# Kernel tuning notes

Hardware: AMD Instinct MI355X
Metric: run time of the kernel (lower is better)

Reference implementation:

```python
import jax, jax.numpy as jnp
import numpy as np

N_CAND = 10   # n_point_candidate
SIGMA = 1.0   # std threshold for vote filtering
EPS = 1e-6


def _get_pt_candidates(pcld, kpts_ofst, seg, cpt_ofst, k):
    # pcld [b,n,3]; kpts_ofst [b,n,8,3]; seg [b,n,1]; cpt_ofst [b,n,1,3]
    offsets = jnp.concatenate([kpts_ofst, cpt_ofst], axis=2)        # [b,n,9,3]
    scores = jnp.squeeze(seg, axis=-1)                              # [b,n]
    _, idx = jax.lax.top_k(scores, k)                               # [b,k] most confident points
    cands = pcld[:, :, None, :] + offsets                           # [b,n,9,3] candidate kpt positions
    cands = jnp.take_along_axis(cands, idx[:, :, None, None], axis=1)  # [b,k,9,3]
    return jnp.transpose(cands, (0, 2, 1, 3))                       # [b,9,k,3]


def _pts_clustering_with_std(kpts_cans, sigma=SIGMA):
    # kpts_cans [b,n_kpts,k,3]: keep candidates within sigma*std of the mean, average survivors
    mean = jnp.mean(kpts_cans, axis=2, keepdims=True)
    std = jnp.std(kpts_cans, axis=2, keepdims=True)
    inlier = jnp.all(jnp.abs(kpts_cans - mean) <= sigma * std, axis=-1)  # [b,n_kpts,k]
    w = inlier.astype(kpts_cans.dtype)[..., None]
    return jnp.sum(kpts_cans * w, axis=2) / (jnp.sum(w, axis=2) + EPS)   # [b,n_kpts,3]


def _rt_svd_transform(A, B, w):
    # Weighted Kabsch: find R,t with R @ A + t ~= B.  A,B [b,n,3]; w [n]
    wn = w / jnp.sum(w)
    cA = jnp.einsum('n,bnc->bc', wn, A)[:, None, :]                 # weighted centroids
    cB = jnp.einsum('n,bnc->bc', wn, B)[:, None, :]
    Am, Bm = A - cA, B - cB
    H = jnp.einsum('bni,n,bnj->bij', Am, w, Bm)                     # [b,3,3] cross-covariance
    U, S, Vh = jnp.linalg.svd(H)
    V = jnp.swapaxes(Vh, -1, -2)
    R0 = V @ jnp.swapaxes(U, -1, -2)
    flip = jnp.where(jnp.linalg.det(R0) < 0.0, -1.0, 1.0)           # reflection fix
    V = V.at[:, :, -1].multiply(flip[:, None])
    R = V @ jnp.swapaxes(U, -1, -2)                                 # [b,3,3]
    t = jnp.swapaxes(cB, -1, -2) - R @ jnp.swapaxes(cA, -1, -2)     # [b,3,1]
    return R, t


def setup_inputs() -> dict:
    key = jax.random.key(0)
    k1, k2, k3, k4, k5 = jax.random.split(key, 5)
    b, n, nk = 64, 12288, 8
    return {
        'pcld_input': jax.random.normal(k1, (b, n, 3), jnp.float32),
        'kpts_pre_input': jax.random.normal(k2, (b, n, nk, 3), jnp.float32),
        'cpt_pre_input': jax.random.normal(k3, (b, n, 1, 3), jnp.float32),
        'seg_pre_input': jax.random.uniform(k4, (b, n, 1), jnp.float32),
        'mesh_kpts_input': jax.random.normal(k5, (b, nk + 1, 3), jnp.float32),
    }


def reference(pcld_input, kpts_pre_input, cpt_pre_input, seg_pre_input, mesh_kpts_input):
    obj_kpts = _get_pt_candidates(pcld_input, kpts_pre_input, seg_pre_input, cpt_pre_input, N_CAND)
    kpts_voted = _pts_clustering_with_std(obj_kpts)                 # [b,9,3]
    n_pts = kpts_voted.shape[1]
    weights_vector = jnp.ones((n_pts,), dtype=kpts_voted.dtype)
    batch_R, batch_t = _rt_svd_transform(mesh_kpts_input, kpts_voted, weights_vector)
    batch_t = jnp.reshape(batch_t, (-1, 3))
    return batch_R, batch_t, kpts_voted
```

## Files before the change

kernel.cpp:

```cpp
#include <hip/hip_runtime.h>
#include <math.h>

typedef unsigned long long u64;
typedef unsigned int u32;

#define NB      64
#define NPTS    12288
#define KTOP    10
#define NKP     9
#define T       1024
#define CAND_MAX 128
#define THETA   0.997f

#define CHUNKS   4
#define TPB_A    768
#define CAP      64
#define TPB_B    128
#define WS_STRIDE 320

__device__ __forceinline__ u64 pack(float v, int idx) {
    return ((u64)__float_as_uint(v) << 32) | (u32)(~idx);
}
__device__ __forceinline__ int unpack_idx(u64 p) { return (int)(~(u32)p); }

__device__ __forceinline__ float rcp_fast(float x)  { return __builtin_amdgcn_rcpf(x); }
__device__ __forceinline__ float rsq_fast(float x)  { return __builtin_amdgcn_rsqf(x); }
__device__ __forceinline__ float sqrt_fast(float x) { return __builtin_amdgcn_sqrtf(x); }

__global__ __launch_bounds__(TPB_A)
void pose_filter(const float* __restrict__ seg, u64* __restrict__ ws)
{
    const int blk   = blockIdx.x;
    const int b     = blk >> 2;
    const int chunk = blk & 3;
    const int t     = threadIdx.x;

    __shared__ u64 lc[CAP];
    __shared__ int lcnt;
    if (t == 0) lcnt = 0;
    __syncthreads();

    const float4* segc4 = (const float4*)(seg + (size_t)b * NPTS) + (size_t)chunk * TPB_A;
    float4 a = segc4[t];
    const int base_idx = chunk * (TPB_A * 4) + t * 4;
    #pragma unroll
    for (int c = 0; c < 4; ++c) {
        float v = (c == 0) ? a.x : (c == 1) ? a.y : (c == 2) ? a.z : a.w;
        if (v >= THETA) {
            int slot = atomicAdd(&lcnt, 1);
            if (slot < CAP) lc[slot] = pack(v, base_idx + c);
        }
    }
    __syncthreads();

    u64* wb = ws + (size_t)b * WS_STRIDE;
    if (t == 0) wb[chunk] = (u64)lcnt;
    int m = lcnt < CAP ? lcnt : CAP;
    if (t < m) wb[4 + chunk * CAP + t] = lc[t];
}

__global__ __launch_bounds__(TPB_B)
void pose_solve(const float* __restrict__ pcld,
                const float* __restrict__ kpts,
                const float* __restrict__ cpt,
                const float* __restrict__ seg,
                const float* __restrict__ mesh,
                const u64*   __restrict__ ws,
                float* __restrict__ out)
{
    const int b = blockIdx.x;
    const int t = threadIdx.x;
    const int lane = t & 63;

    __shared__ u64    cand[CHUNKS * CAP];
    __shared__ int    n_s, bad_s;
    __shared__ int    off_s[CHUNKS];
    __shared__ int    topidx[KTOP];
    __shared__ float4 cands4[NKP][KTOP];
    __shared__ float  voted[NKP][3];
    __shared__ float  meshS[NKP * 3];

    float meshv = 0.0f;
    if (t < NKP * 3) meshv = mesh[(size_t)b * (NKP * 3) + t];

    const u64* wb = ws + (size_t)b * WS_STRIDE;
    if (t == 0) {
        int off = 0, bad = 0;
        #pragma unroll
        for (int c = 0; c < CHUNKS; ++c) {
            int cc = (int)wb[c];
            off_s[c] = off;
            off += cc;
            if (cc > CAP) bad = 1;
        }
        n_s = off;
        bad_s = bad;
    }
    if (t < NKP * 3) meshS[t] = meshv;
    __syncthreads();

    const int n = n_s;
    const int bad = bad_s;

    if (!bad) {
        #pragma unroll
        for (int c = 0; c < CHUNKS; ++c) {
            int o   = off_s[c];
            int cc  = ((c + 1 < CHUNKS) ? off_s[c + 1] : n) - o;
            if (t < cc) cand[o + t] = wb[4 + c * CAP + t];
        }
    }
    __syncthreads();

    if (!bad && n >= KTOP) {
        u64 my0 = (t < n)           ? cand[t]           : 0;
        u64 my1 = (t + TPB_B < n)   ? cand[t + TPB_B]   : 0;
        int r0 = 0, r1 = 0;
        for (int i = 0; i < n; ++i) {
            u64 ci = cand[i];
            r0 += (ci > my0) ? 1 : 0;
            r1 += (ci > my1) ? 1 : 0;
        }
        if (t < n && r0 < KTOP)         topidx[r0] = unpack_idx(my0);
        if (t + TPB_B < n && r1 < KTOP) topidx[r1] = unpack_idx(my1);
    } else if (t < 64) {
        const float* segb = seg + (size_t)b * NPTS;
        u64 loc[KTOP];
        #pragma unroll
        for (int j = 0; j < KTOP; ++j) loc[j] = 0;
        for (int i = lane; i < NPTS; i += 64) {
            u64 p = pack(segb[i], i);
            if (p > loc[KTOP - 1]) {
                loc[KTOP - 1] = p;
                #pragma unroll
                for (int j = KTOP - 1; j > 0; --j) {
                    if (loc[j] > loc[j - 1]) { u64 tmp = loc[j]; loc[j] = loc[j - 1]; loc[j - 1] = tmp; }
                }
            }
        }
        u64 cur = loc[0];
        #pragma unroll
        for (int k = 0; k < KTOP; ++k) {
            u64 w = cur;
            #pragma unroll
            for (int s = 1; s < 64; s <<= 1) {
                u64 o = __shfl_xor(w, s);
                w = o > w ? o : w;
            }
            if (lane == 0) topidx[k] = unpack_idx(w);
            if (cur == w) {
                #pragma unroll
                for (int i = 0; i + 1 < KTOP; ++i) loc[i] = loc[i + 1];
                loc[KTOP - 1] = 0;
                cur = loc[0];
            }
        }
    }
    __syncthreads();

    if (t < NKP * KTOP) {
        int j = t / KTOP;
        int i = t % KTOP;
        int p = topidx[i];
        size_t base = (size_t)b * NPTS + p;
        float px = pcld[base * 3 + 0], py = pcld[base * 3 + 1], pz = pcld[base * 3 + 2];
        float ox, oy, oz;
        if (j < 8) {
            size_t kb = (base * 8 + j) * 3;
            ox = kpts[kb + 0]; oy = kpts[kb + 1]; oz = kpts[kb + 2];
        } else {
            size_t cb = base * 3;
            ox = cpt[cb + 0]; oy = cpt[cb + 1]; oz = cpt[cb + 2];
        }
        cands4[j][i] = make_float4(px + ox, py + oy, pz + oz, 0.0f);
    }
    __syncthreads();

    if (t < NKP) {
        float4 c4[KTOP];
        #pragma unroll
        for (int i = 0; i < KTOP; ++i) c4[i] = cands4[t][i];

        float mean[3] = {0.f, 0.f, 0.f};
        #pragma unroll
        for (int i = 0; i < KTOP; ++i) {
            mean[0] += c4[i].x; mean[1] += c4[i].y; mean[2] += c4[i].z;
        }
        #pragma unroll
        for (int c = 0; c < 3; ++c) mean[c] *= (1.0f / KTOP);

        float var[3] = {0.f, 0.f, 0.f};
        #pragma unroll
        for (int i = 0; i < KTOP; ++i) {
            float d0 = c4[i].x - mean[0]; var[0] += d0 * d0;
            float d1 = c4[i].y - mean[1]; var[1] += d1 * d1;
            float d2 = c4[i].z - mean[2]; var[2] += d2 * d2;
        }
        float sd[3];
        #pragma unroll
        for (int c = 0; c < 3; ++c) sd[c] = sqrtf(var[c] * (1.0f / KTOP));

        float wsum = 0.f, acc[3] = {0.f, 0.f, 0.f};
        #pragma unroll
        for (int i = 0; i < KTOP; ++i) {
            bool in = (fabsf(c4[i].x - mean[0]) <= sd[0]) &&
                      (fabsf(c4[i].y - mean[1]) <= sd[1]) &&
                      (fabsf(c4[i].z - mean[2]) <= sd[2]);
            if (in) {
                wsum += 1.f;
                acc[0] += c4[i].x; acc[1] += c4[i].y; acc[2] += c4[i].z;
            }
        }
        float inv = 1.f / (wsum + 1e-6f);
        #pragma unroll
        for (int c = 0; c < 3; ++c) {
            float v = acc[c] * inv;
            voted[t][c] = v;
            out[NB * 9 + NB * 3 + ((size_t)b * NKP + t) * 3 + c] = v;
        }
    }
    __syncthreads();

    if (t == 0) {
        float A[NKP][3], Bv[NKP][3];
        float cA[3] = {0, 0, 0}, cB[3] = {0, 0, 0};
        for (int nn = 0; nn < NKP; ++nn) {
            for (int c = 0; c < 3; ++c) {
                A[nn][c]  = meshS[nn * 3 + c];
                Bv[nn][c] = voted[nn][c];
                cA[c] += A[nn][c];
                cB[c] += Bv[nn][c];
            }
        }
        for (int c = 0; c < 3; ++c) { cA[c] *= (1.0f / NKP); cB[c] *= (1.0f / NKP); }

        float H[3][3] = {{0,0,0},{0,0,0},{0,0,0}};
        for (int nn = 0; nn < NKP; ++nn)
            for (int i = 0; i < 3; ++i)
                for (int j = 0; j < 3; ++j)
                    H[i][j] += (A[nn][i] - cA[i]) * (Bv[nn][j] - cB[j]);

        float Km[3][3];
        for (int i = 0; i < 3; ++i)
            for (int j = 0; j < 3; ++j) {
                float s = 0;
                for (int l = 0; l < 3; ++l) s += H[l][i] * H[l][j];
                Km[i][j] = s;
            }

        float V[3][3] = {{1,0,0},{0,1,0},{0,0,1}};
        for (int sweep = 0; sweep < 5; ++sweep) {
            for (int p = 0; p < 2; ++p) {
                for (int q = p + 1; q < 3; ++q) {
                    float apq = Km[p][q];
                    float app = Km[p][p], aqq = Km[q][q];
                    if (fabsf(apq) <= 1e-12f * (fabsf(app) + fabsf(aqq)) || apq == 0.0f) continue;
                    float theta = (aqq - app) * rcp_fast(2.0f * apq);
                    float tj = ((theta >= 0.0f) ? 1.0f : -1.0f) *
                               rcp_fast(fabsf(theta) + sqrt_fast(theta * theta + 1.0f));
                    float cj = rsq_fast(tj * tj + 1.0f);
                    float sj = tj * cj;
                    for (int l = 0; l < 3; ++l) {
                        float klp = Km[l][p], klq = Km[l][q];
                        Km[l][p] = cj * klp - sj * klq;
                        Km[l][q] = sj * klp + cj * klq;
                    }
                    for (int l = 0; l < 3; ++l) {
                        float kpl = Km[p][l], kql = Km[q][l];
                        Km[p][l] = cj * kpl - sj * kql;
                        Km[q][l] = sj * kpl + cj * kql;
                    }
                    for (int l = 0; l < 3; ++l) {
                        float vlp = V[l][p], vlq = V[l][q];
                        V[l][p] = cj * vlp - sj * vlq;
                        V[l][q] = sj * vlp + cj * vlq;
                    }
                }
            }
        }

        float eig[3] = {Km[0][0], Km[1][1], Km[2][2]};
        int ord[3] = {0, 1, 2};
        if (eig[ord[0]] < eig[ord[1]]) { int tmp = ord[0]; ord[0] = ord[1]; ord[1] = tmp; }
        if (eig[ord[1]] < eig[ord[2]]) { int tmp = ord[1]; ord[1] = ord[2]; ord[2] = tmp; }
        if (eig[ord[0]] < eig[ord[1]]) { int tmp = ord[0]; ord[0] = ord[1]; ord[1] = tmp; }

        float detH =
            H[0][0] * (H[1][1] * H[2][2] - H[1][2] * H[2][1]) -
            H[0][1] * (H[1][0] * H[2][2] - H[1][2] * H[2][0]) +
            H[0][2] * (H[1][0] * H[2][1] - H[1][1] * H[2][0]);
        float dsign[3] = {1.0f, 1.0f, (detH < 0.0f) ? -1.0f : 1.0f};

        float R[3][3] = {{0,0,0},{0,0,0},{0,0,0}};
        for (int k = 0; k < 3; ++k) {
            int c = ord[k];
            float s = sqrt_fast(fmaxf(eig[c], 0.0f));
            float invs = rcp_fast(fmaxf(s, 1e-12f));
            float u[3];
            for (int l = 0; l < 3; ++l) {
                float a = 0;
                for (int m = 0; m < 3; ++m) a += H[l][m] * V[m][c];
                u[l] = a * invs;
            }
            for (int r = 0; r < 3; ++r)
                for (int cc = 0; cc < 3; ++cc)
                    R[r][cc] += dsign[k] * V[r][c] * u[cc];
        }

        float tv[3];
        for (int c = 0; c < 3; ++c) {
            float a = 0;
            for (int m = 0; m < 3; ++m) a += R[c][m] * cA[m];
            tv[c] = cB[c] - a;
        }

        for (int r = 0; r < 3; ++r)
            for (int c = 0; c < 3; ++c)
                out[(size_t)b * 9 + r * 3 + c] = R[r][c];
        for (int c = 0; c < 3; ++c)
            out[NB * 9 + (size_t)b * 3 + c] = tv[c];
    }
}

__global__ __launch_bounds__(T)
void pose_fused(const float* __restrict__ pcld,
                const float* __restrict__ kpts,
                const float* __restrict__ cpt,
                const float* __restrict__ seg,
                const float* __restrict__ mesh,
                float* __restrict__ out)
{
    const int b = blockIdx.x;
    const int t = threadIdx.x;
    const int lane = t & 63;
    const int wid = t >> 6;

    __shared__ u64    cand[CAND_MAX];
    __shared__ int    cnt;
    __shared__ int    topidx[KTOP];
    __shared__ float4 cands4[NKP][KTOP];
    __shared__ float  voted[NKP][3];
    __shared__ float  meshS[NKP * 3];

    if (t == 0) cnt = 0;
    float meshv = 0.0f;
    if (t < NKP * 3) meshv = mesh[(size_t)b * (NKP * 3) + t];
    __syncthreads();

    const float4* segb4 = (const float4*)(seg + (size_t)b * NPTS);
    #pragma unroll
    for (int j = 0; j < 3; ++j) {
        int f4 = t + j * T;
        float4 a = segb4[f4];
        #pragma unroll
        for (int c = 0; c < 4; ++c) {
            float v = (c == 0) ? a.x : (c == 1) ? a.y : (c == 2) ? a.z : a.w;
            if (v >= THETA) {
                int slot = atomicAdd(&cnt, 1);
                if (slot < CAND_MAX) cand[slot] = pack(v, 4 * f4 + c);
            }
        }
    }
    if (t < NKP * 3) meshS[t] = meshv;
    __syncthreads();

    if (wid == 0) {
        int n = cnt;
        if (n >= KTOP && n <= CAND_MAX) {
            u64 my0 = (lane < n)      ? cand[lane]      : 0;
            u64 my1 = (lane + 64 < n) ? cand[lane + 64] : 0;
            int r0 = 0, r1 = 0;
            for (int i = 0; i < n; ++i) {
                u64 ci = cand[i];
                r0 += (ci > my0) ? 1 : 0;
                r1 += (ci > my1) ? 1 : 0;
            }
            if (lane < n && r0 < KTOP)      topidx[r0] = unpack_idx(my0);
            if (lane + 64 < n && r1 < KTOP) topidx[r1] = unpack_idx(my1);
        } else {
            const float* segb = seg + (size_t)b * NPTS;
            u64 loc[KTOP];
            #pragma unroll
            for (int j = 0; j < KTOP; ++j) loc[j] = 0;
            for (int i = lane; i < NPTS; i += 64) {
                u64 p = pack(segb[i], i);
                if (p > loc[KTOP - 1]) {
                    loc[KTOP - 1] = p;
                    #pragma unroll
                    for (int j = KTOP - 1; j > 0; --j) {
                        if (loc[j] > loc[j - 1]) { u64 tmp = loc[j]; loc[j] = loc[j - 1]; loc[j - 1] = tmp; }
                    }
                }
            }
            u64 cur = loc[0];
            #pragma unroll
            for (int k = 0; k < KTOP; ++k) {
                u64 w = cur;
                #pragma unroll
                for (int s = 1; s < 64; s <<= 1) {
                    u64 o = __shfl_xor(w, s);
                    w = o > w ? o : w;
                }
                if (lane == 0) topidx[k] = unpack_idx(w);
                if (cur == w) {
                    #pragma unroll
                    for (int i = 0; i + 1 < KTOP; ++i) loc[i] = loc[i + 1];
                    loc[KTOP - 1] = 0;
                    cur = loc[0];
                }
            }
        }
    }
    __syncthreads();

    if (t < NKP * KTOP) {
        int j = t / KTOP;
        int i = t % KTOP;
        int p = topidx[i];
        size_t base = (size_t)b * NPTS + p;
        float px = pcld[base * 3 + 0], py = pcld[base * 3 + 1], pz = pcld[base * 3 + 2];
        float ox, oy, oz;
        if (j < 8) {
            size_t kb = (base * 8 + j) * 3;
            ox = kpts[kb + 0]; oy = kpts[kb + 1]; oz = kpts[kb + 2];
        } else {
            size_t cb = base * 3;
            ox = cpt[cb + 0]; oy = cpt[cb + 1]; oz = cpt[cb + 2];
        }
        cands4[j][i] = make_float4(px + ox, py + oy, pz + oz, 0.0f);
    }
    __syncthreads();

    if (t < NKP) {
        float4 c4[KTOP];
        #pragma unroll
        for (int i = 0; i < KTOP; ++i) c4[i] = cands4[t][i];
        float mean[3] = {0.f, 0.f, 0.f};
        #pragma unroll
        for (int i = 0; i < KTOP; ++i) { mean[0] += c4[i].x; mean[1] += c4[i].y; mean[2] += c4[i].z; }
        #pragma unroll
        for (int c = 0; c < 3; ++c) mean[c] *= (1.0f / KTOP);
        float var[3] = {0.f, 0.f, 0.f};
        #pragma unroll
        for (int i = 0; i < KTOP; ++i) {
            float d0 = c4[i].x - mean[0]; var[0] += d0 * d0;
            float d1 = c4[i].y - mean[1]; var[1] += d1 * d1;
            float d2 = c4[i].z - mean[2]; var[2] += d2 * d2;
        }
        float sd[3];
        #pragma unroll
        for (int c = 0; c < 3; ++c) sd[c] = sqrtf(var[c] * (1.0f / KTOP));
        float wsum = 0.f, acc[3] = {0.f, 0.f, 0.f};
        #pragma unroll
        for (int i = 0; i < KTOP; ++i) {
            bool in = (fabsf(c4[i].x - mean[0]) <= sd[0]) &&
                      (fabsf(c4[i].y - mean[1]) <= sd[1]) &&
                      (fabsf(c4[i].z - mean[2]) <= sd[2]);
            if (in) { wsum += 1.f; acc[0] += c4[i].x; acc[1] += c4[i].y; acc[2] += c4[i].z; }
        }
        float inv = 1.f / (wsum + 1e-6f);
        #pragma unroll
        for (int c = 0; c < 3; ++c) {
            float v = acc[c] * inv;
            voted[t][c] = v;
            out[NB * 9 + NB * 3 + ((size_t)b * NKP + t) * 3 + c] = v;
        }
    }
    __syncthreads();

    if (t == 0) {
        float A[NKP][3], Bv[NKP][3];
        float cA[3] = {0, 0, 0}, cB[3] = {0, 0, 0};
        for (int nn = 0; nn < NKP; ++nn) {
            for (int c = 0; c < 3; ++c) {
                A[nn][c]  = meshS[nn * 3 + c];
                Bv[nn][c] = voted[nn][c];
                cA[c] += A[nn][c];
                cB[c] += Bv[nn][c];
            }
        }
        for (int c = 0; c < 3; ++c) { cA[c] *= (1.0f / NKP); cB[c] *= (1.0f / NKP); }
        float H[3][3] = {{0,0,0},{0,0,0},{0,0,0}};
        for (int nn = 0; nn < NKP; ++nn)
            for (int i = 0; i < 3; ++i)
                for (int j = 0; j < 3; ++j)
                    H[i][j] += (A[nn][i] - cA[i]) * (Bv[nn][j] - cB[j]);
        float Km[3][3];
        for (int i = 0; i < 3; ++i)
            for (int j = 0; j < 3; ++j) {
                float s = 0;
                for (int l = 0; l < 3; ++l) s += H[l][i] * H[l][j];
                Km[i][j] = s;
            }
        float V[3][3] = {{1,0,0},{0,1,0},{0,0,1}};
        for (int sweep = 0; sweep < 5; ++sweep) {
            for (int p = 0; p < 2; ++p) {
                for (int q = p + 1; q < 3; ++q) {
                    float apq = Km[p][q];
                    float app = Km[p][p], aqq = Km[q][q];
                    if (fabsf(apq) <= 1e-12f * (fabsf(app) + fabsf(aqq)) || apq == 0.0f) continue;
                    float theta = (aqq - app) * rcp_fast(2.0f * apq);
                    float tj = ((theta >= 0.0f) ? 1.0f : -1.0f) *
                               rcp_fast(fabsf(theta) + sqrt_fast(theta * theta + 1.0f));
                    float cj = rsq_fast(tj * tj + 1.0f);
                    float sj = tj * cj;
                    for (int l = 0; l < 3; ++l) {
                        float klp = Km[l][p], klq = Km[l][q];
                        Km[l][p] = cj * klp - sj * klq;
                        Km[l][q] = sj * klp + cj * klq;
                    }
                    for (int l = 0; l < 3; ++l) {
                        float kpl = Km[p][l], kql = Km[q][l];
                        Km[p][l] = cj * kpl - sj * kql;
                        Km[q][l] = sj * kpl + cj * kql;
                    }
                    for (int l = 0; l < 3; ++l) {
                        float vlp = V[l][p], vlq = V[l][q];
                        V[l][p] = cj * vlp - sj * vlq;
                        V[l][q] = sj * vlp + cj * vlq;
                    }
                }
            }
        }
        float eig[3] = {Km[0][0], Km[1][1], Km[2][2]};
        int ord[3] = {0, 1, 2};
        if (eig[ord[0]] < eig[ord[1]]) { int tmp = ord[0]; ord[0] = ord[1]; ord[1] = tmp; }
        if (eig[ord[1]] < eig[ord[2]]) { int tmp = ord[1]; ord[1] = ord[2]; ord[2] = tmp; }
        if (eig[ord[0]] < eig[ord[1]]) { int tmp = ord[0]; ord[0] = ord[1]; ord[1] = tmp; }
        float detH =
            H[0][0] * (H[1][1] * H[2][2] - H[1][2] * H[2][1]) -
            H[0][1] * (H[1][0] * H[2][2] - H[1][2] * H[2][0]) +
            H[0][2] * (H[1][0] * H[2][1] - H[1][1] * H[2][0]);
        float dsign[3] = {1.0f, 1.0f, (detH < 0.0f) ? -1.0f : 1.0f};
        float R[3][3] = {{0,0,0},{0,0,0},{0,0,0}};
        for (int k = 0; k < 3; ++k) {
            int c = ord[k];
            float s = sqrt_fast(fmaxf(eig[c], 0.0f));
            float invs = rcp_fast(fmaxf(s, 1e-12f));
            float u[3];
            for (int l = 0; l < 3; ++l) {
                float a = 0;
                for (int m = 0; m < 3; ++m) a += H[l][m] * V[m][c];
                u[l] = a * invs;
            }
            for (int r = 0; r < 3; ++r)
                for (int cc = 0; cc < 3; ++cc)
                    R[r][cc] += dsign[k] * V[r][c] * u[cc];
        }
        float tv[3];
        for (int c = 0; c < 3; ++c) {
            float a = 0;
            for (int m = 0; m < 3; ++m) a += R[c][m] * cA[m];
            tv[c] = cB[c] - a;
        }
        for (int r = 0; r < 3; ++r)
            for (int c = 0; c < 3; ++c)
                out[(size_t)b * 9 + r * 3 + c] = R[r][c];
        for (int c = 0; c < 3; ++c)
            out[NB * 9 + (size_t)b * 3 + c] = tv[c];
    }
}

extern "C" void kernel_launch(void* const* d_in, const int* in_sizes, int n_in,
                              void* d_out, int out_size, void* d_ws, size_t ws_size,
                              hipStream_t stream) {
    const float* pcld = (const float*)d_in[0];
    const float* kpts = (const float*)d_in[1];
    const float* cpt  = (const float*)d_in[2];
    const float* seg  = (const float*)d_in[3];
    const float* mesh = (const float*)d_in[4];
    float* out = (float*)d_out;

    const size_t need = (size_t)NB * WS_STRIDE * sizeof(u64);
    if (d_ws != nullptr && ws_size >= need) {
        u64* ws = (u64*)d_ws;
        pose_filter<<<NB * CHUNKS, TPB_A, 0, stream>>>(seg, ws);
        pose_solve<<<NB, TPB_B, 0, stream>>>(pcld, kpts, cpt, seg, mesh, ws, out);
    } else {
        pose_fused<<<NB, T, 0, stream>>>(pcld, kpts, cpt, seg, mesh, out);
    }
}
```

Baseline: 120.2 us.

## Merge filter and solve kernels using last-block-done atomic counter

The filter and solve kernels are fused into one launch. Each of the four chunk blocks per batch writes its threshold candidates to workspace, then bumps a per-batch atomic counter, and the last block to arrive runs the top-k, voting and SVD solve. This removes the second kernel launch and its dependency gap. In exchange it adds a memset of the counters before every launch, thread fences, and a solve stage that runs in a 768-thread block where only a few threads do work. The rank computation now skips empty slots using per-chunk counts instead of compacting the candidates first.

```diff
diff --git a/kernel.cpp b/kernel.cpp
--- a/kernel.cpp
+++ b/kernel.cpp
@@ -15,7 +15,6 @@
 #define CHUNKS   4
 #define TPB_A    768
 #define CAP      64
-#define TPB_B    128
 #define WS_STRIDE 320
 
 __device__ __forceinline__ u64 pack(float v, int idx) {
@@ -28,15 +27,32 @@
 __device__ __forceinline__ float sqrt_fast(float x) { return __builtin_amdgcn_sqrtf(x); }
 
 __global__ __launch_bounds__(TPB_A)
-void pose_filter(const float* __restrict__ seg, u64* __restrict__ ws)
+void pose_onepass(const float* __restrict__ pcld,
+                  const float* __restrict__ kpts,
+                  const float* __restrict__ cpt,
+                  const float* __restrict__ seg,
+                  const float* __restrict__ mesh,
+                  u32* __restrict__ ctr,
+                  u64* __restrict__ wsd,
+                  float* __restrict__ out)
 {
     const int blk   = blockIdx.x;
     const int b     = blk >> 2;
     const int chunk = blk & 3;
     const int t     = threadIdx.x;
-
-    __shared__ u64 lc[CAP];
-    __shared__ int lcnt;
+    const int lane  = t & 63;
+
+    __shared__ u64    lc[CAP];
+    __shared__ int    lcnt;
+    __shared__ int    last_s;
+    __shared__ u64    cand[CHUNKS * CAP];
+    __shared__ int    cnts_s[CHUNKS];
+    __shared__ int    n_s, bad_s;
+    __shared__ int    topidx[KTOP];
+    __shared__ float4 cands4[NKP][KTOP];
+    __shared__ float  voted[NKP][3];
+    __shared__ float  meshS[NKP * 3];
+
     if (t == 0) lcnt = 0;
     __syncthreads();
 
@@ -53,48 +69,35 @@
     }
     __syncthreads();
 
-    u64* wb = ws + (size_t)b * WS_STRIDE;
+    u64* wb = wsd + (size_t)b * WS_STRIDE;
     if (t == 0) wb[chunk] = (u64)lcnt;
     int m = lcnt < CAP ? lcnt : CAP;
     if (t < m) wb[4 + chunk * CAP + t] = lc[t];
-}
-
-__global__ __launch_bounds__(TPB_B)
-void pose_solve(const float* __restrict__ pcld,
-                const float* __restrict__ kpts,
-                const float* __restrict__ cpt,
-                const float* __restrict__ seg,
-                const float* __restrict__ mesh,
-                const u64*   __restrict__ ws,
-                float* __restrict__ out)
-{
-    const int b = blockIdx.x;
-    const int t = threadIdx.x;
-    const int lane = t & 63;
-
-    __shared__ u64    cand[CHUNKS * CAP];
-    __shared__ int    n_s, bad_s;
-    __shared__ int    off_s[CHUNKS];
-    __shared__ int    topidx[KTOP];
-    __shared__ float4 cands4[NKP][KTOP];
-    __shared__ float  voted[NKP][3];
-    __shared__ float  meshS[NKP * 3];
+    __syncthreads();
+
+    if (t == 0) {
+        __threadfence();
+        u32 old = atomicAdd(&ctr[b], 1u);
+        if (old == 3u) __threadfence();
+        last_s = (old == 3u) ? 1 : 0;
+    }
+    __syncthreads();
+    if (!last_s) return;
 
     float meshv = 0.0f;
     if (t < NKP * 3) meshv = mesh[(size_t)b * (NKP * 3) + t];
-
-    const u64* wb = ws + (size_t)b * WS_STRIDE;
+    if (t < CHUNKS * CAP) cand[t] = wb[4 + t];
     if (t == 0) {
-        int off = 0, bad = 0;
+        int off = 0, badv = 0;
         #pragma unroll
         for (int c = 0; c < CHUNKS; ++c) {
             int cc = (int)wb[c];
-            off_s[c] = off;
+            cnts_s[c] = cc < CAP ? cc : CAP;
             off += cc;
-            if (cc > CAP) bad = 1;
+            if (cc > CAP) badv = 1;
         }
         n_s = off;
-        bad_s = bad;
+        bad_s = badv;
     }
     if (t < NKP * 3) meshS[t] = meshv;
     __syncthreads();
@@ -102,27 +105,19 @@
     const int n = n_s;
     const int bad = bad_s;
 
-    if (!bad) {
-        #pragma unroll
-        for (int c = 0; c < CHUNKS; ++c) {
-            int o   = off_s[c];
-            int cc  = ((c + 1 < CHUNKS) ? off_s[c + 1] : n) - o;
-            if (t < cc) cand[o + t] = wb[4 + c * CAP + t];
-        }
-    }
-    __syncthreads();
-
     if (!bad && n >= KTOP) {
-        u64 my0 = (t < n)           ? cand[t]           : 0;
-        u64 my1 = (t + TPB_B < n)   ? cand[t + TPB_B]   : 0;
-        int r0 = 0, r1 = 0;
-        for (int i = 0; i < n; ++i) {
-            u64 ci = cand[i];
-            r0 += (ci > my0) ? 1 : 0;
-            r1 += (ci > my1) ? 1 : 0;
-        }
-        if (t < n && r0 < KTOP)         topidx[r0] = unpack_idx(my0);
-        if (t + TPB_B < n && r1 < KTOP) topidx[r1] = unpack_idx(my1);
+        if (t < CHUNKS * CAP) {
+            u64 my = cand[t];
+            bool valid = (t & (CAP - 1)) < cnts_s[t >> 6];
+            int r = 0;
+            #pragma unroll
+            for (int c2 = 0; c2 < CHUNKS; ++c2) {
+                int cc = cnts_s[c2];
+                for (int i2 = 0; i2 < cc; ++i2)
+                    r += (cand[c2 * CAP + i2] > my) ? 1 : 0;
+            }
+            if (valid && r < KTOP) topidx[r] = unpack_idx(my);
+        }
     } else if (t < 64) {
         const float* segb = seg + (size_t)b * NPTS;
         u64 loc[KTOP];
@@ -298,9 +293,9 @@
             float invs = rcp_fast(fmaxf(s, 1e-12f));
             float u[3];
             for (int l = 0; l < 3; ++l) {
-                float a = 0;
-                for (int m = 0; m < 3; ++m) a += H[l][m] * V[m][c];
-                u[l] = a * invs;
+                float a2 = 0;
+                for (int mm = 0; mm < 3; ++mm) a2 += H[l][mm] * V[mm][c];
+                u[l] = a2 * invs;
             }
             for (int r = 0; r < 3; ++r)
                 for (int cc = 0; cc < 3; ++cc)
@@ -309,9 +304,9 @@
 
         float tv[3];
         for (int c = 0; c < 3; ++c) {
-            float a = 0;
-            for (int m = 0; m < 3; ++m) a += R[c][m] * cA[m];
-            tv[c] = cB[c] - a;
+            float a2 = 0;
+            for (int mm = 0; mm < 3; ++mm) a2 += R[c][mm] * cA[mm];
+            tv[c] = cB[c] - a2;
         }
 
         for (int r = 0; r < 3; ++r)
@@ -539,9 +534,9 @@
             float invs = rcp_fast(fmaxf(s, 1e-12f));
             float u[3];
             for (int l = 0; l < 3; ++l) {
-                float a = 0;
-                for (int m = 0; m < 3; ++m) a += H[l][m] * V[m][c];
-                u[l] = a * invs;
+                float a2 = 0;
+                for (int mm = 0; mm < 3; ++mm) a2 += H[l][mm] * V[mm][c];
+                u[l] = a2 * invs;
             }
             for (int r = 0; r < 3; ++r)
                 for (int cc = 0; cc < 3; ++cc)
@@ -549,9 +544,9 @@
         }
         float tv[3];
         for (int c = 0; c < 3; ++c) {
-            float a = 0;
-            for (int m = 0; m < 3; ++m) a += R[c][m] * cA[m];
-            tv[c] = cB[c] - a;
+            float a2 = 0;
+            for (int mm = 0; mm < 3; ++mm) a2 += R[c][mm] * cA[mm];
+            tv[c] = cB[c] - a2;
         }
         for (int r = 0; r < 3; ++r)
             for (int c = 0; c < 3; ++c)
@@ -571,11 +566,12 @@
     const float* mesh = (const float*)d_in[4];
     float* out = (float*)d_out;
 
-    const size_t need = (size_t)NB * WS_STRIDE * sizeof(u64);
+    const size_t need = 256 + (size_t)NB * WS_STRIDE * sizeof(u64);
     if (d_ws != nullptr && ws_size >= need) {
-        u64* ws = (u64*)d_ws;
-        pose_filter<<<NB * CHUNKS, TPB_A, 0, stream>>>(seg, ws);
-        pose_solve<<<NB, TPB_B, 0, stream>>>(pcld, kpts, cpt, seg, mesh, ws, out);
+        u32* ctr = (u32*)d_ws;
+        u64* wsd = (u64*)((char*)d_ws + 256);
+        hipMemsetAsync(d_ws, 0, NB * sizeof(u32), stream);
+        pose_onepass<<<NB * CHUNKS, TPB_A, 0, stream>>>(pcld, kpts, cpt, seg, mesh, ctr, wsd, out);
     } else {
         pose_fused<<<NB, T, 0, stream>>>(pcld, kpts, cpt, seg, mesh, out);
     }
```

Result: slower. 133.3 us (+10.9%).
